# Kernel optimization log

Hardware: AMD Instinct MI355X
Metric: run time of the kernel (lower is better)

## Reference

```python
import jax, jax.numpy as jnp
import numpy as np

B, T, P, D, L = 16, 120, 96, 128, 2


def setup_inputs() -> dict:
    key = jax.random.key(0)
    k1, k2, k3, k4 = jax.random.split(key, 4)
    x = jax.random.normal(k1, (B, P, D, T), dtype=jnp.float32)
    # distances: symmetric-ish positive pairwise distances from random 3D points
    pts = jax.random.uniform(k2, (B, T, P, 3), dtype=jnp.float32) * 5.0
    diff = pts[:, :, :, None, :] - pts[:, :, None, :, :]
    distances = jnp.sqrt(jnp.sum(diff * diff, axis=-1) + 1e-12)
    # contiguous-prefix padding mask (matches the original self-loop loop semantics)
    counts = jax.random.randint(k3, (B,), P // 2, P + 1)
    padding_mask = jnp.arange(P)[None, :] < counts[:, None]
    # params: xavier_uniform with gain 1e-5 ~ tiny; bias 0; LN gamma=1, beta=0
    limit = 1e-5 * np.sqrt(6.0 / (D + D))
    W = jax.random.uniform(k4, (L, D, D), minval=-limit, maxval=limit, dtype=jnp.float32)
    b = jnp.zeros((L, D), dtype=jnp.float32)
    gamma = jnp.ones((L, D), dtype=jnp.float32)
    beta = jnp.zeros((L, D), dtype=jnp.float32)
    return {"x": x, "distances": distances, "padding_mask": padding_mask,
            "W": W, "b": b, "gamma": gamma, "beta": beta}


def _build_adjacency(distances, padding_mask):
    # valid_mask: [B,T,P,P]
    vm2d = (padding_mask[:, :, None] & padding_mask[:, None, :]).astype(distances.dtype)  # [B,P,P]
    vm = vm2d[:, None, :, :]
    vd = distances * vm
    pos = (vd > 0).astype(distances.dtype)
    n = jnp.sum(pos)
    mean = jnp.sum(vd * pos) / n
    var = jnp.sum(((vd - mean) ** 2) * pos) / (n - 1.0)  # unbiased, as torch.std
    sigma = jnp.sqrt(var) + 1e-8
    adj = jnp.exp(-(distances ** 2) / (2.0 * sigma ** 2)) * vm
    # self loops on valid (contiguous-prefix) nodes: add diag(mask)
    eye_mask = jnp.eye(P, dtype=distances.dtype)[None, :, :] * padding_mask[:, :, None].astype(distances.dtype)
    adj = adj + eye_mask[:, None, :, :]
    # symmetric normalization D^{-1/2} A D^{-1/2}
    deg = jnp.clip(jnp.sum(adj, axis=-1, keepdims=True), 1e-8, None)  # [B,T,P,1]
    deg = jnp.clip(deg * padding_mask[:, None, :, None].astype(distances.dtype), 1e-8, None)
    dis = deg ** -0.5
    adj = dis * adj * jnp.swapaxes(dis, -2, -1)
    return adj * vm


def _layer_norm_D(x, g, bt, eps=1e-5):
    # x: [B,P,D,T]; normalize over D axis
    mu = jnp.mean(x, axis=2, keepdims=True)
    var = jnp.mean((x - mu) ** 2, axis=2, keepdims=True)
    return (x - mu) * jax.lax.rsqrt(var + eps) * g[None, None, :, None] + bt[None, None, :, None]


def reference(x, distances, padding_mask, W, b, gamma, beta):
    adj = _build_adjacency(distances, padding_mask)  # [B,T,P,P]
    mask_f = padding_mask.astype(x.dtype)
    for l in range(L):
        xt = jnp.transpose(x, (0, 3, 1, 2))                      # [B,T,P,D]
        h = jnp.einsum('btpd,de->btpe', xt, W[l])                # x @ W
        o = jnp.einsum('btpq,btqd->btpd', adj, h)                # A @ xW
        o = jax.nn.relu(o + b[l])
        o = o * mask_f[:, None, :, None]
        o = jnp.transpose(o, (0, 2, 3, 1))                       # [B,P,D,T]
        o = _layer_norm_D(o, gamma[l], beta[l])
        x = x + o
    return x
```

## Files before the change

### kernel.cpp

```cpp
#include <hip/hip_runtime.h>
#include <math.h>

typedef __bf16 bf16_t;
typedef __bf16 bf16x8 __attribute__((ext_vector_type(8)));
typedef __bf16 bf16x4 __attribute__((ext_vector_type(4)));
typedef float f32x4 __attribute__((ext_vector_type(4)));

namespace {
constexpr int kB = 16;
constexpr int kT = 120;
constexpr int kP = 96;
constexpr int kD = 128;
constexpr int kBT = kB * kT;
constexpr int kPP = kP * kP;
constexpr int kPD = kP * kD;
constexpr long long kND = (long long)kBT * kPP;

constexpr int YS = 136;
constexpr int HS = 104;
constexpr int OS = 132;
constexpr int AS = 104;
constexpr int UNION_B = 26624;
constexpr int AL_OFF = UNION_B;
constexpr int MROW_OFF = AL_OFF + 19968;
constexpr int SMEM_B = MROW_OFF + 384;
}

__device__ __forceinline__ f32x4 mfma16(bf16x8 a, bf16x8 b, f32x4 c) {
    return __builtin_amdgcn_mfma_f32_16x16x32_bf16(a, b, c, 0, 0, 0);
}

__global__ void k_mask(const unsigned char* __restrict__ mraw, int* __restrict__ mask,
                       double* __restrict__ stats) {
    int tid = threadIdx.x;
    if (tid < 4) stats[tid] = 0.0;
    const unsigned int* u32 = (const unsigned int*)mraw;
    unsigned int w0 = u32[0];
    int mode;
    if (w0 == 0x01010101u) mode = 0;
    else if (w0 == 1u) mode = 1;
    else mode = 2;
    for (int i = tid; i < kB * kP; i += blockDim.x) {
        int v;
        if (mode == 0)      v = (mraw[i] != 0);
        else if (mode == 1) v = (u32[i] != 0);
        else                v = (((const float*)mraw)[i] != 0.0f);
        mask[i] = v;
    }
}

__global__ void k_prep(const float* __restrict__ W, bf16_t* __restrict__ wT) {
    int l = blockIdx.y;
    int idx = blockIdx.x * 256 + threadIdx.x;
    int n = idx >> 7, k = idx & 127;
    wT[l * 16384 + n * 128 + k] = (bf16_t)W[l * 16384 + k * 128 + n];
}

__global__ __launch_bounds__(256) void k_stats(const float* __restrict__ dist,
                                               const int* __restrict__ mask,
                                               double* __restrict__ stats) {
    __shared__ int ml[kB * kP];
    for (int i = threadIdx.x; i < kB * kP; i += 256) ml[i] = mask[i];
    __syncthreads();

    long long n4 = kND / 4;
    long long stride = (long long)gridDim.x * 256;
    double s = 0.0, s2 = 0.0;
    int cnt = 0;
    for (long long i4 = (long long)blockIdx.x * 256 + threadIdx.x; i4 < n4; i4 += stride) {
        int q0 = 4 * (int)(i4 % 24);
        long long r = i4 / 24;
        int p = (int)(r % 96);
        int b = (int)((r / 96) / kT);
        const int* mb = ml + b * kP;
        if (mb[p]) {
            float4 d4 = *(const float4*)(dist + i4 * 4);
            if (mb[q0 + 0]) { s += d4.x; s2 += (double)d4.x * d4.x; cnt++; }
            if (mb[q0 + 1]) { s += d4.y; s2 += (double)d4.y * d4.y; cnt++; }
            if (mb[q0 + 2]) { s += d4.z; s2 += (double)d4.z * d4.z; cnt++; }
            if (mb[q0 + 3]) { s += d4.w; s2 += (double)d4.w * d4.w; cnt++; }
        }
    }
    __shared__ double sh[256];
    int tid = threadIdx.x;
    sh[tid] = s; __syncthreads();
    for (int off = 128; off > 0; off >>= 1) { if (tid < off) sh[tid] += sh[tid + off]; __syncthreads(); }
    if (tid == 0) atomicAdd(&stats[0], sh[0]);
    __syncthreads();
    sh[tid] = s2; __syncthreads();
    for (int off = 128; off > 0; off >>= 1) { if (tid < off) sh[tid] += sh[tid + off]; __syncthreads(); }
    if (tid == 0) atomicAdd(&stats[1], sh[0]);
    __syncthreads();
    sh[tid] = (double)cnt; __syncthreads();
    for (int off = 128; off > 0; off >>= 1) { if (tid < off) sh[tid] += sh[tid + off]; __syncthreads(); }
    if (tid == 0) atomicAdd(&stats[2], sh[0]);
}

__global__ void k_fin(const double* __restrict__ stats, float* __restrict__ params) {
    double n = stats[2];
    double mean = stats[0] / n;
    double var = (stats[1] - n * mean * mean) / (n - 1.0);
    double sigma = sqrt(var) + 1e-8;
    params[0] = (float)(1.0 / (2.0 * sigma * sigma));
}

__global__ __launch_bounds__(256) void k_adj(const float* __restrict__ dist,
                                             const int* __restrict__ mask,
                                             const float* __restrict__ params,
                                             bf16_t* __restrict__ adj) {
    __shared__ float aT[kP * 100];
    __shared__ float dis[kP];
    __shared__ float mr[kP];
    int bt = blockIdx.x;
    int b = bt / kT;
    int tid = threadIdx.x;
    if (tid < kP) mr[tid] = (float)mask[b * kP + tid];
    float inv2s2 = params[0];
    __syncthreads();
    const float* dbt = dist + (long long)bt * kPP;
    #pragma unroll
    for (int k = 0; k < 9; ++k) {
        int i4 = k * 256 + tid;
        int e = i4 * 4;
        int p = e / kP, q = e - p * kP;
        float4 d4 = *(const float4*)(dbt + e);
        float mp = mr[p];
        float v[4];
        v[0] = mp * mr[q + 0] != 0.f ? __expf(-d4.x * d4.x * inv2s2) : 0.f;
        v[1] = mp * mr[q + 1] != 0.f ? __expf(-d4.y * d4.y * inv2s2) : 0.f;
        v[2] = mp * mr[q + 2] != 0.f ? __expf(-d4.z * d4.z * inv2s2) : 0.f;
        v[3] = mp * mr[q + 3] != 0.f ? __expf(-d4.w * d4.w * inv2s2) : 0.f;
        #pragma unroll
        for (int j = 0; j < 4; ++j) {
            if (p == q + j) v[j] += mp;
            aT[p * 100 + q + j] = v[j];
        }
    }
    __syncthreads();
    if (tid < kP) {
        float s = 0.f;
        for (int q = 0; q < kP; ++q) s += aT[q * 100 + tid];
        s = fmaxf(s, 1e-8f);
        s = fmaxf(s * mr[tid], 1e-8f);
        dis[tid] = rsqrtf(s);
    }
    __syncthreads();
    bf16_t* obt = adj + (long long)bt * kPP;
    #pragma unroll
    for (int k = 0; k < 9; ++k) {
        int i4 = k * 256 + tid;
        int e = i4 * 4;
        int p = e / kP, q = e - p * kP;
        float dp = dis[p];
        bf16x4 ov;
        #pragma unroll
        for (int j = 0; j < 4; ++j)
            ov[j] = (bf16_t)(dp * aT[p * 100 + q + j] * dis[q + j]);
        *(bf16x4*)(obt + e) = ov;
    }
}

__global__ __launch_bounds__(256) void k_tin(const float* __restrict__ x,
                                             bf16_t* __restrict__ y) {
    __shared__ float tile[64 * 121];
    int b = blockIdx.y, pd0 = blockIdx.x * 64;
    int tid = threadIdx.x;
    const float* xb = x + ((long long)b * kPD + pd0) * kT;
    #pragma unroll
    for (int k = 0; k < 8; ++k) {
        int idx = k * 256 + tid;
        if (idx < 1920) {
            int r = idx / 30, c = idx - r * 30;
            float4 v = *(const float4*)(xb + r * kT + c * 4);
            tile[r * 121 + c * 4 + 0] = v.x;
            tile[r * 121 + c * 4 + 1] = v.y;
            tile[r * 121 + c * 4 + 2] = v.z;
            tile[r * 121 + c * 4 + 3] = v.w;
        }
    }
    __syncthreads();
    bf16_t* yb = y + (long long)b * kT * kPD + pd0;
    #pragma unroll
    for (int k = 0; k < 4; ++k) {
        int idx = k * 256 + tid;
        if (idx < 960) {
            int t = idx >> 3, dg = idx & 7;
            bf16x8 o;
            #pragma unroll
            for (int j = 0; j < 8; ++j) o[j] = (bf16_t)tile[(dg * 8 + j) * 121 + t];
            *(bf16x8*)(yb + (long long)t * kPD + dg * 8) = o;
        }
    }
}

__global__ __launch_bounds__(256) void k_tout(const bf16_t* __restrict__ y,
                                              float* __restrict__ out) {
    __shared__ float tile[64 * 121];
    int b = blockIdx.y, pd0 = blockIdx.x * 64;
    int tid = threadIdx.x;
    const bf16_t* yb = y + (long long)b * kT * kPD + pd0;
    #pragma unroll
    for (int k = 0; k < 4; ++k) {
        int idx = k * 256 + tid;
        if (idx < 960) {
            int t = idx >> 3, dg = idx & 7;
            bf16x8 v = *(const bf16x8*)(yb + (long long)t * kPD + dg * 8);
            #pragma unroll
            for (int j = 0; j < 8; ++j) tile[(dg * 8 + j) * 121 + t] = (float)v[j];
        }
    }
    __syncthreads();
    float* ob = out + ((long long)b * kPD + pd0) * kT;
    #pragma unroll
    for (int k = 0; k < 8; ++k) {
        int idx = k * 256 + tid;
        if (idx < 1920) {
            int r = idx / 30, c = idx - r * 30;
            float4 v;
            v.x = tile[r * 121 + c * 4 + 0];
            v.y = tile[r * 121 + c * 4 + 1];
            v.z = tile[r * 121 + c * 4 + 2];
            v.w = tile[r * 121 + c * 4 + 3];
            *(float4*)(ob + r * kT + c * 4) = v;
        }
    }
}

__global__ __launch_bounds__(256, 3) void k_gcn(bf16_t* __restrict__ y,
                                                const bf16_t* __restrict__ adj,
                                                const int* __restrict__ mask,
                                                const bf16_t* __restrict__ wT,
                                                const float* __restrict__ bias,
                                                const float* __restrict__ gamma,
                                                const float* __restrict__ beta) {
    __shared__ __align__(16) char smem[SMEM_B];
    bf16_t* yL  = (bf16_t*)smem;
    bf16_t* hT  = (bf16_t*)smem;
    bf16_t* oLb = (bf16_t*)smem;
    bf16_t* aL  = (bf16_t*)(smem + AL_OFF);
    float* mrowf = (float*)(smem + MROW_OFF);

    const int tid = threadIdx.x;
    const int tx = tid & 15, ty = tid >> 4;
    const int lane = tid & 63, w = tid >> 6;
    const int fc = lane & 15, fg = lane >> 4;
    const int bt = blockIdx.x, b = bt / kT;
    const int d0 = tx * 8;

    bf16_t* ybt = y + (size_t)bt * kPD;
    const bf16_t* abt = adj + (size_t)bt * kPP;

    if (tid < kP) mrowf[tid] = (float)mask[b * kP + tid];

    #pragma unroll
    for (int k = 0; k < 9; ++k) {
        int e4 = (k * 256 + tid) * 4;
        int p = e4 / kP, q = e4 - p * kP;
        *(bf16x4*)(aL + p * AS + q) = *(const bf16x4*)(abt + e4);
    }

    float res[6][8];
    #pragma unroll
    for (int i = 0; i < 6; ++i) {
        int p = ty * 6 + i;
        bf16x8 v = *(const bf16x8*)(ybt + p * kD + d0);
        #pragma unroll
        for (int j = 0; j < 8; ++j) res[i][j] = (float)v[j];
        *(bf16x8*)(yL + p * YS + d0) = v;
    }

    for (int l = 0; l < 2; ++l) {
        const bf16_t* wTl = wT + l * kD * kD;
        bf16x8 wf[4][2];
        #pragma unroll
        for (int kt = 0; kt < 4; ++kt) {
            wf[kt][0] = *(const bf16x8*)(wTl + (w * 32 + fc) * kD + kt * 32 + fg * 8);
            wf[kt][1] = *(const bf16x8*)(wTl + (w * 32 + 16 + fc) * kD + kt * 32 + fg * 8);
        }
        __syncthreads();

        f32x4 acc[6][2];
        #pragma unroll
        for (int mt = 0; mt < 6; ++mt) { acc[mt][0] = {0,0,0,0}; acc[mt][1] = {0,0,0,0}; }
        #pragma unroll
        for (int kt = 0; kt < 4; ++kt) {
            #pragma unroll
            for (int mt = 0; mt < 6; ++mt) {
                bf16x8 af = *(const bf16x8*)(yL + (mt * 16 + fc) * YS + kt * 32 + fg * 8);
                acc[mt][0] = mfma16(af, wf[kt][0], acc[mt][0]);
                acc[mt][1] = mfma16(af, wf[kt][1], acc[mt][1]);
            }
        }
        __syncthreads();

        #pragma unroll
        for (int mt = 0; mt < 6; ++mt)
            #pragma unroll
            for (int nn = 0; nn < 2; ++nn) {
                int e = (w * 2 + nn) * 16 + fc;
                int p0 = mt * 16 + fg * 4;
                bf16x4 hv = {(bf16_t)acc[mt][nn][0], (bf16_t)acc[mt][nn][1],
                             (bf16_t)acc[mt][nn][2], (bf16_t)acc[mt][nn][3]};
                *(bf16x4*)(hT + e * HS + p0) = hv;
            }
        __syncthreads();

        f32x4 acc2[6][2];
        #pragma unroll
        for (int mt = 0; mt < 6; ++mt) { acc2[mt][0] = {0,0,0,0}; acc2[mt][1] = {0,0,0,0}; }
        #pragma unroll
        for (int kt = 0; kt < 3; ++kt) {
            bf16x8 bf0 = *(const bf16x8*)(hT + (w * 32 + fc) * HS + kt * 32 + fg * 8);
            bf16x8 bf1 = *(const bf16x8*)(hT + (w * 32 + 16 + fc) * HS + kt * 32 + fg * 8);
            #pragma unroll
            for (int mt = 0; mt < 6; ++mt) {
                bf16x8 af = *(const bf16x8*)(aL + (mt * 16 + fc) * AS + kt * 32 + fg * 8);
                acc2[mt][0] = mfma16(af, bf0, acc2[mt][0]);
                acc2[mt][1] = mfma16(af, bf1, acc2[mt][1]);
            }
        }
        __syncthreads();

        #pragma unroll
        for (int mt = 0; mt < 6; ++mt)
            #pragma unroll
            for (int nn = 0; nn < 2; ++nn) {
                int d = (w * 2 + nn) * 16 + fc;
                int p0 = mt * 16 + fg * 4;
                oLb[(p0 + 0) * OS + d] = (bf16_t)acc2[mt][nn][0];
                oLb[(p0 + 1) * OS + d] = (bf16_t)acc2[mt][nn][1];
                oLb[(p0 + 2) * OS + d] = (bf16_t)acc2[mt][nn][2];
                oLb[(p0 + 3) * OS + d] = (bf16_t)acc2[mt][nn][3];
            }
        __syncthreads();

        const float* bl = bias + l * kD;
        const float* gl = gamma + l * kD;
        const float* bel = beta + l * kD;
        float4 bb0 = *(const float4*)(bl + d0), bb1 = *(const float4*)(bl + d0 + 4);
        float4 gg0 = *(const float4*)(gl + d0), gg1 = *(const float4*)(gl + d0 + 4);
        float4 be0 = *(const float4*)(bel + d0), be1 = *(const float4*)(bel + d0 + 4);
        float bb[8] = {bb0.x, bb0.y, bb0.z, bb0.w, bb1.x, bb1.y, bb1.z, bb1.w};
        float gg[8] = {gg0.x, gg0.y, gg0.z, gg0.w, gg1.x, gg1.y, gg1.z, gg1.w};
        float be[8] = {be0.x, be0.y, be0.z, be0.w, be1.x, be1.y, be1.z, be1.w};

        #pragma unroll
        for (int i = 0; i < 6; ++i) {
            int p = ty * 6 + i;
            float mpf = mrowf[p];
            bf16x4 o0 = *(const bf16x4*)(oLb + p * OS + d0);
            bf16x4 o1 = *(const bf16x4*)(oLb + p * OS + d0 + 4);
            float v[8];
            #pragma unroll
            for (int j = 0; j < 4; ++j) {
                v[j]     = fmaxf((float)o0[j] + bb[j], 0.f) * mpf;
                v[j + 4] = fmaxf((float)o1[j] + bb[j + 4], 0.f) * mpf;
            }
            float s = v[0] + v[1] + v[2] + v[3] + v[4] + v[5] + v[6] + v[7];
            s += __shfl_xor(s, 8);
            s += __shfl_xor(s, 4);
            s += __shfl_xor(s, 2);
            s += __shfl_xor(s, 1);
            float mu = s * 0.0078125f;

            float ss = 0.f;
            #pragma unroll
            for (int j = 0; j < 8; ++j) { float dv = v[j] - mu; ss += dv * dv; }
            ss += __shfl_xor(ss, 8);
            ss += __shfl_xor(ss, 4);
            ss += __shfl_xor(ss, 2);
            ss += __shfl_xor(ss, 1);
            float inv = rsqrtf(ss * 0.0078125f + 1e-5f);

            #pragma unroll
            for (int j = 0; j < 8; ++j)
                res[i][j] += (v[j] - mu) * inv * gg[j] + be[j];
        }

        if (l == 0) {
            __syncthreads();
            #pragma unroll
            for (int i = 0; i < 6; ++i) {
                int p = ty * 6 + i;
                bf16x8 c;
                #pragma unroll
                for (int j = 0; j < 8; ++j) c[j] = (bf16_t)res[i][j];
                *(bf16x8*)(yL + p * YS + d0) = c;
            }
        } else {
            #pragma unroll
            for (int i = 0; i < 6; ++i) {
                int p = ty * 6 + i;
                bf16x8 c;
                #pragma unroll
                for (int j = 0; j < 8; ++j) c[j] = (bf16_t)res[i][j];
                *(bf16x8*)(ybt + p * kD + d0) = c;
            }
        }
    }
}

extern "C" void kernel_launch(void* const* d_in, const int* in_sizes, int n_in,
                              void* d_out, int out_size, void* d_ws, size_t ws_size,
                              hipStream_t stream) {
    (void)in_sizes; (void)n_in; (void)out_size; (void)ws_size;

    const float* x = (const float*)d_in[0];
    const float* dist = (const float*)d_in[1];
    const unsigned char* mraw = (const unsigned char*)d_in[2];
    const float* W = (const float*)d_in[3];
    const float* bias = (const float*)d_in[4];
    const float* gamma = (const float*)d_in[5];
    const float* beta = (const float*)d_in[6];
    float* out = (float*)d_out;

    char* ws = (char*)d_ws;
    double* stats = (double*)ws;
    float* params = (float*)(ws + 32);
    int* mask = (int*)(ws + 64);
    bf16_t* wT = (bf16_t*)(ws + 8192);
    bf16_t* adj = (bf16_t*)(ws + 81920);
    bf16_t* y = (bf16_t*)(ws + 81920 + (size_t)kBT * kPP * 2);

    k_mask<<<1, 256, 0, stream>>>(mraw, mask, stats);
    k_prep<<<dim3(64, 2), 256, 0, stream>>>(W, wT);
    k_stats<<<1024, 256, 0, stream>>>(dist, mask, stats);
    k_fin<<<1, 1, 0, stream>>>(stats, params);
    k_adj<<<kBT, 256, 0, stream>>>(dist, mask, params, adj);

    k_tin<<<dim3(kPD / 64, kB), 256, 0, stream>>>(x, y);

    k_gcn<<<kBT, 256, 0, stream>>>(y, adj, mask, wT, bias, gamma, beta);

    k_tout<<<dim3(kPD / 64, kB), 256, 0, stream>>>(y, out);
}
```

Measured before the change: 192.5 us.

## Double GCN block to 512 threads and keep residual in bf16 registers

The fused GCN kernel now runs 512 threads per block. Eight waves are arranged as a 2x4 grid over output rows and columns, so each wave handles 3 M-tiles instead of 6, and each thread owns 3 rows instead of 6 in the LayerNorm/residual stage. The fp32 residual array is replaced by bf16 register vectors, which cuts register pressure to allow higher occupancy. The cost is rounding the residual to bf16 after layer 0, which adds some precision loss, and more barrier participants per block.

```diff
diff --git a/kernel.cpp b/kernel.cpp
--- a/kernel.cpp
+++ b/kernel.cpp
@@ -226,7 +226,7 @@
     }
 }
 
-__global__ __launch_bounds__(256, 3) void k_gcn(bf16_t* __restrict__ y,
+__global__ __launch_bounds__(512, 5) void k_gcn(bf16_t* __restrict__ y,
                                                 const bf16_t* __restrict__ adj,
                                                 const int* __restrict__ mask,
                                                 const bf16_t* __restrict__ wT,
@@ -243,6 +243,7 @@
     const int tid = threadIdx.x;
     const int tx = tid & 15, ty = tid >> 4;
     const int lane = tid & 63, w = tid >> 6;
+    const int wm = w >> 2, wn = w & 3;
     const int fc = lane & 15, fg = lane >> 4;
     const int bt = blockIdx.x, b = bt / kT;
     const int d0 = tx * 8;
@@ -253,20 +254,21 @@
     if (tid < kP) mrowf[tid] = (float)mask[b * kP + tid];
 
     #pragma unroll
-    for (int k = 0; k < 9; ++k) {
-        int e4 = (k * 256 + tid) * 4;
-        int p = e4 / kP, q = e4 - p * kP;
-        *(bf16x4*)(aL + p * AS + q) = *(const bf16x4*)(abt + e4);
-    }
-
-    float res[6][8];
-    #pragma unroll
-    for (int i = 0; i < 6; ++i) {
-        int p = ty * 6 + i;
-        bf16x8 v = *(const bf16x8*)(ybt + p * kD + d0);
-        #pragma unroll
-        for (int j = 0; j < 8; ++j) res[i][j] = (float)v[j];
-        *(bf16x8*)(yL + p * YS + d0) = v;
+    for (int k = 0; k < 5; ++k) {
+        int i4 = k * 512 + tid;
+        if (i4 < 2304) {
+            int e4 = i4 * 4;
+            int p = e4 / kP, q = e4 - p * kP;
+            *(bf16x4*)(aL + p * AS + q) = *(const bf16x4*)(abt + e4);
+        }
+    }
+
+    bf16x8 yR[3];
+    #pragma unroll
+    for (int i = 0; i < 3; ++i) {
+        int p = ty * 3 + i;
+        yR[i] = *(const bf16x8*)(ybt + p * kD + d0);
+        *(bf16x8*)(yL + p * YS + d0) = yR[i];
     }
 
     for (int l = 0; l < 2; ++l) {
@@ -274,19 +276,19 @@
         bf16x8 wf[4][2];
         #pragma unroll
         for (int kt = 0; kt < 4; ++kt) {
-            wf[kt][0] = *(const bf16x8*)(wTl + (w * 32 + fc) * kD + kt * 32 + fg * 8);
-            wf[kt][1] = *(const bf16x8*)(wTl + (w * 32 + 16 + fc) * kD + kt * 32 + fg * 8);
+            wf[kt][0] = *(const bf16x8*)(wTl + ((wn * 2 + 0) * 16 + fc) * kD + kt * 32 + fg * 8);
+            wf[kt][1] = *(const bf16x8*)(wTl + ((wn * 2 + 1) * 16 + fc) * kD + kt * 32 + fg * 8);
         }
         __syncthreads();
 
-        f32x4 acc[6][2];
-        #pragma unroll
-        for (int mt = 0; mt < 6; ++mt) { acc[mt][0] = {0,0,0,0}; acc[mt][1] = {0,0,0,0}; }
+        f32x4 acc[3][2];
+        #pragma unroll
+        for (int mt = 0; mt < 3; ++mt) { acc[mt][0] = {0,0,0,0}; acc[mt][1] = {0,0,0,0}; }
         #pragma unroll
         for (int kt = 0; kt < 4; ++kt) {
             #pragma unroll
-            for (int mt = 0; mt < 6; ++mt) {
-                bf16x8 af = *(const bf16x8*)(yL + (mt * 16 + fc) * YS + kt * 32 + fg * 8);
+            for (int mt = 0; mt < 3; ++mt) {
+                bf16x8 af = *(const bf16x8*)(yL + ((wm * 3 + mt) * 16 + fc) * YS + kt * 32 + fg * 8);
                 acc[mt][0] = mfma16(af, wf[kt][0], acc[mt][0]);
                 acc[mt][1] = mfma16(af, wf[kt][1], acc[mt][1]);
             }
@@ -294,27 +296,27 @@
         __syncthreads();
 
         #pragma unroll
-        for (int mt = 0; mt < 6; ++mt)
+        for (int mt = 0; mt < 3; ++mt)
             #pragma unroll
             for (int nn = 0; nn < 2; ++nn) {
-                int e = (w * 2 + nn) * 16 + fc;
-                int p0 = mt * 16 + fg * 4;
+                int e = (wn * 2 + nn) * 16 + fc;
+                int p0 = (wm * 3 + mt) * 16 + fg * 4;
                 bf16x4 hv = {(bf16_t)acc[mt][nn][0], (bf16_t)acc[mt][nn][1],
                              (bf16_t)acc[mt][nn][2], (bf16_t)acc[mt][nn][3]};
                 *(bf16x4*)(hT + e * HS + p0) = hv;
             }
         __syncthreads();
 
-        f32x4 acc2[6][2];
-        #pragma unroll
-        for (int mt = 0; mt < 6; ++mt) { acc2[mt][0] = {0,0,0,0}; acc2[mt][1] = {0,0,0,0}; }
+        f32x4 acc2[3][2];
+        #pragma unroll
+        for (int mt = 0; mt < 3; ++mt) { acc2[mt][0] = {0,0,0,0}; acc2[mt][1] = {0,0,0,0}; }
         #pragma unroll
         for (int kt = 0; kt < 3; ++kt) {
-            bf16x8 bf0 = *(const bf16x8*)(hT + (w * 32 + fc) * HS + kt * 32 + fg * 8);
-            bf16x8 bf1 = *(const bf16x8*)(hT + (w * 32 + 16 + fc) * HS + kt * 32 + fg * 8);
-            #pragma unroll
-            for (int mt = 0; mt < 6; ++mt) {
-                bf16x8 af = *(const bf16x8*)(aL + (mt * 16 + fc) * AS + kt * 32 + fg * 8);
+            bf16x8 bf0 = *(const bf16x8*)(hT + ((wn * 2 + 0) * 16 + fc) * HS + kt * 32 + fg * 8);
+            bf16x8 bf1 = *(const bf16x8*)(hT + ((wn * 2 + 1) * 16 + fc) * HS + kt * 32 + fg * 8);
+            #pragma unroll
+            for (int mt = 0; mt < 3; ++mt) {
+                bf16x8 af = *(const bf16x8*)(aL + ((wm * 3 + mt) * 16 + fc) * AS + kt * 32 + fg * 8);
                 acc2[mt][0] = mfma16(af, bf0, acc2[mt][0]);
                 acc2[mt][1] = mfma16(af, bf1, acc2[mt][1]);
             }
@@ -322,11 +324,11 @@
         __syncthreads();
 
         #pragma unroll
-        for (int mt = 0; mt < 6; ++mt)
+        for (int mt = 0; mt < 3; ++mt)
             #pragma unroll
             for (int nn = 0; nn < 2; ++nn) {
-                int d = (w * 2 + nn) * 16 + fc;
-                int p0 = mt * 16 + fg * 4;
+                int d = (wn * 2 + nn) * 16 + fc;
+                int p0 = (wm * 3 + mt) * 16 + fg * 4;
                 oLb[(p0 + 0) * OS + d] = (bf16_t)acc2[mt][nn][0];
                 oLb[(p0 + 1) * OS + d] = (bf16_t)acc2[mt][nn][1];
                 oLb[(p0 + 2) * OS + d] = (bf16_t)acc2[mt][nn][2];
@@ -345,8 +347,8 @@
         float be[8] = {be0.x, be0.y, be0.z, be0.w, be1.x, be1.y, be1.z, be1.w};
 
         #pragma unroll
-        for (int i = 0; i < 6; ++i) {
-            int p = ty * 6 + i;
+        for (int i = 0; i < 3; ++i) {
+            int p = ty * 3 + i;
             float mpf = mrowf[p];
             bf16x4 o0 = *(const bf16x4*)(oLb + p * OS + d0);
             bf16x4 o1 = *(const bf16x4*)(oLb + p * OS + d0 + 4);
@@ -372,30 +374,22 @@
             ss += __shfl_xor(ss, 1);
             float inv = rsqrtf(ss * 0.0078125f + 1e-5f);
 
+            bf16x8 c;
             #pragma unroll
             for (int j = 0; j < 8; ++j)
-                res[i][j] += (v[j] - mu) * inv * gg[j] + be[j];
+                c[j] = (bf16_t)((float)yR[i][j] + (v[j] - mu) * inv * gg[j] + be[j]);
+            yR[i] = c;
         }
 
         if (l == 0) {
             __syncthreads();
             #pragma unroll
-            for (int i = 0; i < 6; ++i) {
-                int p = ty * 6 + i;
-                bf16x8 c;
-                #pragma unroll
-                for (int j = 0; j < 8; ++j) c[j] = (bf16_t)res[i][j];
-                *(bf16x8*)(yL + p * YS + d0) = c;
-            }
+            for (int i = 0; i < 3; ++i)
+                *(bf16x8*)(yL + (ty * 3 + i) * YS + d0) = yR[i];
         } else {
             #pragma unroll
-            for (int i = 0; i < 6; ++i) {
-                int p = ty * 6 + i;
-                bf16x8 c;
-                #pragma unroll
-                for (int j = 0; j < 8; ++j) c[j] = (bf16_t)res[i][j];
-                *(bf16x8*)(ybt + p * kD + d0) = c;
-            }
+            for (int i = 0; i < 3; ++i)
+                *(bf16x8*)(ybt + (ty * 3 + i) * kD + d0) = yR[i];
         }
     }
 }
@@ -430,7 +424,7 @@
 
     k_tin<<<dim3(kPD / 64, kB), 256, 0, stream>>>(x, y);
 
-    k_gcn<<<kBT, 256, 0, stream>>>(y, adj, mask, wT, bias, gamma, beta);
+    k_gcn<<<kBT, 512, 0, stream>>>(y, adj, mask, wT, bias, gamma, beta);
 
     k_tout<<<dim3(kPD / 64, kB), 256, 0, stream>>>(y, out);
 }
```

After: 212.3 us. +10.3%, slower.
